# Kernel tuning notes

Measured on AMD Instinct MI355X. Metric: run time of the kernel, lower is better.

## Reference

```python
import jax, jax.numpy as jnp
import numpy as np

EPS = 1e-05  # matches tf entropy epsilon


def setup_inputs() -> dict:
    key = jax.random.key(0)
    k1, k2 = jax.random.split(key)
    encodings = jax.random.normal(k1, (8192, 64), dtype=jnp.float32)
    categorical = jax.random.uniform(k2, (8192, 25), dtype=jnp.float32)
    return {"encodings": encodings, "categorical": categorical, "k": 15}


def reference(encodings, categorical, k):
    B = encodings.shape[0]
    n_components = categorical.shape[1]
    k = min(k, B // 4)  # layer clamps k to batch_size // 4

    hard_groups = jnp.argmax(categorical, axis=1)           # [B] int
    max_groups = jnp.max(categorical, axis=1)               # [B]

    # Batched brute-force kNN. tf.norm's sqrt is monotonic, so the strict
    # comparison `dist < kth_dist` is identical on squared distances; working
    # in squared space avoids sqrt(0) issues and an extra pass.
    sq = jnp.sum(encodings * encodings, axis=1)             # [B]
    d2 = sq[:, None] + sq[None, :] - 2.0 * (encodings @ encodings.T)
    d2 = jnp.maximum(d2, 0.0)                               # [B, B]

    # (k+1)-smallest distances per row (0-indexed k, self-distance included,
    # matching tf.gather(tf.sort(distances), k)).
    neg_topk, _ = jax.lax.top_k(-d2, k + 1)                 # [B, k+1]
    kth = -neg_topk[:, k]                                   # [B] k-th smallest

    mask = (d2 < kth[:, None]).astype(jnp.float32)          # [B, B] strict <

    # Per-row label histogram over the neighborhood: counts[i,c] = #neighbors
    # of i in cluster c. Zero bins contribute 0 to -sum(b*log(b+eps)), same as
    # tf.bincount's variable-length output.
    onehot = jax.nn.one_hot(hard_groups, n_components, dtype=jnp.float32)
    counts = mask @ onehot                                  # [B, n_components]
    n_i = jnp.sum(counts, axis=-1, keepdims=True)           # [B, 1]
    bins = counts / jnp.maximum(n_i, 1.0)
    neighbourhood_entropy = -jnp.sum(bins * jnp.log(bins + EPS), axis=-1)  # [B]

    # Global cluster-size entropy + number of populated clusters.
    gcounts = jnp.sum(onehot, axis=0)                       # [n_components]
    gbins = gcounts / jnp.float32(B)
    cluster_size_entropy = -jnp.sum(gbins * jnp.log(gbins + EPS))
    n_populated = jnp.sum(gcounts > 0).astype(jnp.float32)

    return encodings, neighbourhood_entropy, cluster_size_entropy, n_populated, max_groups
```

## Files before the change

### kernel.cpp

```cpp
#include <hip/hip_runtime.h>
#include <math.h>

#define Bsz    8192
#define Dd     64
#define NC     25
#define RT     16
#define KCAP   16
#define EPSf   1e-5f
#define JMASK  2097151

typedef short  short8  __attribute__((ext_vector_type(8)));
typedef float  floatx4 __attribute__((ext_vector_type(4)));


__device__ inline unsigned short f2bf(float x) {
    unsigned u = __float_as_uint(x);
    u += 0x7FFFu + ((u >> 16) & 1u);
    return (unsigned short)(u >> 16);
}
__device__ inline float bf2f(unsigned short h) { return __uint_as_float(((unsigned)h) << 16); }

__device__ inline void oesort16(unsigned* a) {
    #pragma unroll
    for (int p = 1; p < 16; p <<= 1) {
        #pragma unroll
        for (int k = p; k >= 1; k >>= 1) {
            #pragma unroll
            for (int j = (k & (p - 1)); j + k < 16; j += 2 * k) {
                #pragma unroll
                for (int i = 0; i < k; ++i) {
                    if (i + j + k < 16 &&
                        ((i + j) / (2 * p)) == ((i + j + k) / (2 * p))) {
                        unsigned x = a[i + j], y = a[i + j + k];
                        a[i + j]     = (x < y) ? x : y;
                        a[i + j + k] = (x < y) ? y : x;
                    }
                }
            }
        }
    }
}
__device__ inline void bclean16(unsigned* t) {
    #pragma unroll
    for (int j = 8; j > 0; j >>= 1)
        #pragma unroll
        for (int i = 0; i < 16; ++i) {
            int l = i ^ j;
            if (l > i) {
                unsigned x = t[i], y = t[l];
                t[i] = (x < y) ? x : y;
                t[l] = (x < y) ? y : x;
            }
        }
}
__device__ inline void bmerge16(unsigned* ls, const unsigned* b) {
    unsigned t[16];
    #pragma unroll
    for (int i = 0; i < 16; ++i) { unsigned x = ls[i], y = b[15 - i]; t[i] = (x < y) ? x : y; }
    bclean16(t);
    #pragma unroll
    for (int i = 0; i < 16; ++i) ls[i] = t[i];
}
__device__ inline void bmerge16_shfl(unsigned* ls, int mask) {
    unsigned t[16];
    #pragma unroll
    for (int i = 0; i < 16; ++i) {
        unsigned pv = (unsigned)__shfl_xor((int)ls[15 - i], mask);
        unsigned x = ls[i];
        t[i] = (x < pv) ? x : pv;
    }
    bclean16(t);
    #pragma unroll
    for (int i = 0; i < 16; ++i) ls[i] = t[i];
}

struct TileR { short8 a0, a1, a2, a3; uint4 sv; };

__device__ __attribute__((always_inline)) inline void tile_load(
    TileR& T, const char* __restrict__ enc2, const unsigned* __restrict__ slab,
    int soff, int lane16, int quad4)
{
    const char* base = enc2 + soff + lane16;
    T.a0 = *(const short8*)(base);
    T.a1 = *(const short8*)(base + 1024);
    T.a2 = *(const short8*)(base + 2048);
    T.a3 = *(const short8*)(base + 3072);
    T.sv = *(const uint4*)(slab + (soff >> 8) + quad4);
}

__device__ __attribute__((always_inline)) inline void tile_mfma(
    const TileR& T, const short8* bh, const short8* bl, float sqi, unsigned* cand)
{
    floatx4 acc = (floatx4){0.f, 0.f, 0.f, 0.f};
    acc = __builtin_amdgcn_mfma_f32_16x16x32_bf16(T.a0, bh[0], acc, 0, 0, 0);
    acc = __builtin_amdgcn_mfma_f32_16x16x32_bf16(T.a0, bl[0], acc, 0, 0, 0);
    acc = __builtin_amdgcn_mfma_f32_16x16x32_bf16(T.a2, bh[0], acc, 0, 0, 0);
    acc = __builtin_amdgcn_mfma_f32_16x16x32_bf16(T.a1, bh[1], acc, 0, 0, 0);
    acc = __builtin_amdgcn_mfma_f32_16x16x32_bf16(T.a1, bl[1], acc, 0, 0, 0);
    acc = __builtin_amdgcn_mfma_f32_16x16x32_bf16(T.a3, bh[1], acc, 0, 0, 0);

    unsigned s[4] = {T.sv.x, T.sv.y, T.sv.z, T.sv.w};
    #pragma unroll
    for (int r = 0; r < 4; ++r) {
        float d2 = fmaxf(sqi + __uint_as_float(s[r] & ~31u) + acc[r], 0.f);
        cand[r] = (__float_as_uint(d2) & ~31u) | (s[r] & 31u);
    }
}


__global__ __launch_bounds__(256) void pre_kernel(
    const float* __restrict__ enc, const float* __restrict__ cat,
    unsigned int* __restrict__ slab,
    char* __restrict__ enc1, char* __restrict__ enc2,
    float* __restrict__ out_max, float* __restrict__ out_enc)
{
    const int gid = blockIdx.x * 256 + threadIdx.x;
    const int p = gid >> 5, pr = gid & 31;

    float2 ev = ((const float2*)enc)[gid];
    ((float2*)out_enc)[gid] = ev;

    float s = ev.x * ev.x + ev.y * ev.y;
    #pragma unroll
    for (int m = 1; m < 32; m <<= 1) s += __shfl_xor(s, m, 32);

    {
        const int g = p >> 4, c15p = p & 15;
        const int d0 = 2 * pr, kh = d0 >> 5, q = (d0 >> 3) & 3, e0 = d0 & 7;
        const int base = g * 4096 + kh * 1024 + (q * 16 + c15p) * 16 + e0 * 2;
        unsigned short ha = f2bf(ev.x), hb = f2bf(ev.y);
        unsigned short la = f2bf(ev.x - bf2f(ha)), lb = f2bf(ev.y - bf2f(hb));
        *(unsigned*)(enc1 + base)        = (unsigned)ha | ((unsigned)hb << 16);
        *(unsigned*)(enc1 + base + 2048) = (unsigned)la | ((unsigned)lb << 16);
        float y0 = -2.f * ev.x, y1 = -2.f * ev.y;
        unsigned short hc = f2bf(y0), hd = f2bf(y1);
        unsigned short lc = f2bf(y0 - bf2f(hc)), ld = f2bf(y1 - bf2f(hd));
        *(unsigned*)(enc2 + base)        = (unsigned)hc | ((unsigned)hd << 16);
        *(unsigned*)(enc2 + base + 2048) = (unsigned)lc | ((unsigned)ld << 16);
    }
    float cv = (pr < NC) ? cat[p * NC + pr] : -1.f;
    int ci = pr;
    #pragma unroll
    for (int m = 1; m < 32; m <<= 1) {
        float ov = __shfl_xor(cv, m, 32);
        int   oi = __shfl_xor(ci, m, 32);
        if (ov > cv || (ov == cv && oi < ci)) { cv = ov; ci = oi; }
    }
    if (pr == 0) {
        out_max[p] = cv;
        slab[p] = (__float_as_uint(s) & ~31u) | (unsigned)ci;
    }
}

__global__ __launch_bounds__(512) void main_kernel(
    const char* __restrict__ enc1, const char* __restrict__ enc2,
    const unsigned int* __restrict__ slab, const int* __restrict__ kptr,
    float* __restrict__ out_ent, float* __restrict__ out_glob)
{
    __shared__ unsigned wl[8 * 16 * 17];
    __shared__ int cnt[32];

    const int tid  = threadIdx.x, bid = blockIdx.x;
    const int wv   = tid >> 6, lane = tid & 63;
    const int quad = (tid >> 4) & 3, c15 = tid & 15;
    const int rowbase = bid * RT;
    const int lane16 = lane * 16, quad4 = quad * 4;

    short8 bh[2], bl[2];
    {
        const char* ib = enc1 + (size_t)bid * 4096 + lane16;
        bh[0] = *(const short8*)(ib);
        bh[1] = *(const short8*)(ib + 1024);
        bl[0] = *(const short8*)(ib + 2048);
        bl[1] = *(const short8*)(ib + 3072);
    }
    const float sqi = __uint_as_float(slab[rowbase + c15] & ~31u);

    unsigned ls[KCAP];
    #pragma unroll
    for (int q = 0; q < KCAP; ++q) ls[q] = 0xFFFFFFFFu;

    const int wvoff = wv * 4096;

    TileR A0, A1, B0, B1;
    tile_load(A0, enc2, slab, wvoff,          lane16, quad4);
    tile_load(A1, enc2, slab, wvoff + 32768,  lane16, quad4);

    #pragma unroll 1
    for (int p = 0; p < 32; p += 2) {
        unsigned cand[16];
        {
            const int o = (wvoff + (p + 1) * 65536) & JMASK;
            tile_load(B0, enc2, slab, o, lane16, quad4);
        }
        __builtin_amdgcn_sched_barrier(0);
        tile_mfma(A0, bh, bl, sqi, cand);
        {
            const int o = ((wvoff + (p + 1) * 65536) & JMASK) + 32768;
            tile_load(B1, enc2, slab, o, lane16, quad4);
        }
        __builtin_amdgcn_sched_barrier(0);
        tile_mfma(A1, bh, bl, sqi, cand + 4);
        {
            const int o = (wvoff + (p + 2) * 65536) & JMASK;
            tile_load(A0, enc2, slab, o, lane16, quad4);
        }
        __builtin_amdgcn_sched_barrier(0);
        tile_mfma(B0, bh, bl, sqi, cand + 8);
        {
            const int o = ((wvoff + (p + 2) * 65536) & JMASK) + 32768;
            tile_load(A1, enc2, slab, o, lane16, quad4);
        }
        __builtin_amdgcn_sched_barrier(0);
        tile_mfma(B1, bh, bl, sqi, cand + 12);
        oesort16(cand);
        bmerge16(ls, cand);
    }

    if (bid == 0) {
        if (tid < 32) cnt[tid] = 0;
        __syncthreads();
        for (int i = tid; i < Bsz; i += 512) atomicAdd(&cnt[slab[i] & 31u], 1);
        __syncthreads();
        if (tid == 0) {
            float gent = 0.f, npop = 0.f;
            for (int i = 0; i < NC; ++i) {
                int g = cnt[i];
                if (g > 0) {
                    npop += 1.f;
                    float gb = (float)g / (float)Bsz;
                    gent -= gb * logf(gb + EPSf);
                }
            }
            out_glob[0] = gent;
            out_glob[1] = npop;
        }
        __syncthreads();
    }

    bmerge16_shfl(ls, 16);
    bmerge16_shfl(ls, 32);
    if (quad == 0) {
        #pragma unroll
        for (int q = 0; q < KCAP; ++q) wl[(wv * 16 + c15) * 17 + q] = ls[q];
    }
    __syncthreads();
    if (wv == 0) {
        const int row = tid >> 2, sub = tid & 3;
        unsigned A[16], Bv[16];
        #pragma unroll
        for (int i = 0; i < 16; ++i) A[i]  = wl[((2 * sub)     * 16 + row) * 17 + i];
        #pragma unroll
        for (int i = 0; i < 16; ++i) Bv[i] = wl[((2 * sub + 1) * 16 + row) * 17 + i];
        bmerge16(A, Bv);
        bmerge16_shfl(A, 1);
        bmerge16_shfl(A, 2);

        int kk = kptr[0];
        if (kk > Bsz / 4) kk = Bsz / 4;
        if (kk > KCAP - 1) kk = KCAP - 1;

        unsigned kth = A[15];
        #pragma unroll
        for (int q = 0; q < 16; ++q) if (q == kk) kth = A[q];
        int nn = 0;
        #pragma unroll
        for (int t = 0; t < 15; ++t) nn += (t < kk && A[t] < kth) ? 1 : 0;

        float inv = 1.f / (float)((nn > 0) ? nn : 1);
        float part = 0.f;
        #pragma unroll
        for (int a4 = 0; a4 < 4; ++a4) {
            int a = sub + 4 * a4;
            if (a < nn) {
                int la = (int)(A[a] & 31u);
                int c = 0;
                #pragma unroll
                for (int b = 0; b < 15; ++b) c += (b < nn && (int)(A[b] & 31u) == la) ? 1 : 0;
                part -= inv * logf((float)c * inv + EPSf);
            }
        }
        part += __shfl_xor(part, 1);
        part += __shfl_xor(part, 2);
        if (sub == 0) out_ent[rowbase + row] = part;
    }
}

extern "C" void kernel_launch(void* const* d_in, const int* in_sizes, int n_in,
                              void* d_out, int out_size, void* d_ws, size_t ws_size,
                              hipStream_t stream)
{
    const float* enc  = (const float*)d_in[0];
    const float* cat  = (const float*)d_in[1];
    const int*   kptr = (const int*)d_in[2];
    float* out = (float*)d_out;

    unsigned int* slab = (unsigned int*)d_ws;
    char*         enc1 = (char*)d_ws + 32768;
    char*         enc2 = (char*)d_ws + 2129920;

    float* out_enc  = out;
    float* out_ent  = out + Bsz * Dd;
    float* out_glob = out + Bsz * Dd + Bsz;
    float* out_max  = out + Bsz * Dd + Bsz + 2;

    pre_kernel<<<1024, 256, 0, stream>>>(enc, cat, slab, enc1, enc2, out_max, out_enc);
    main_kernel<<<Bsz / RT, 512, 0, stream>>>(enc1, enc2, slab, kptr, out_ent, out_glob);
}
```

Measured before the change: 120.1 us.

## Split squared-norm/label slab, drop clamp via signed keys, stagger wave start offsets

Splits the packed norm+label slab into separate float and label arrays, so the inner loop no longer masks the low bits of the norm. It also drops the fmaxf clamp by switching the sort keys to signed ints, which order negative distances correctly. Each wave now starts at a rotated column offset and sleeps briefly before its first load, to spread memory traffic across waves. The cost is an extra vector load per tile and small startup sleeps.

```diff
diff --git a/kernel.cpp b/kernel.cpp
--- a/kernel.cpp
+++ b/kernel.cpp
@@ -8,6 +8,7 @@
 #define KCAP   16
 #define EPSf   1e-5f
 #define JMASK  2097151
+#define SENT   0x7FFFFFFF
 
 typedef short  short8  __attribute__((ext_vector_type(8)));
 typedef float  floatx4 __attribute__((ext_vector_type(4)));
@@ -20,7 +21,7 @@
 }
 __device__ inline float bf2f(unsigned short h) { return __uint_as_float(((unsigned)h) << 16); }
 
-__device__ inline void oesort16(unsigned* a) {
+__device__ inline void oesort16(int* a) {
     #pragma unroll
     for (int p = 1; p < 16; p <<= 1) {
         #pragma unroll
@@ -31,7 +32,7 @@
                 for (int i = 0; i < k; ++i) {
                     if (i + j + k < 16 &&
                         ((i + j) / (2 * p)) == ((i + j + k) / (2 * p))) {
-                        unsigned x = a[i + j], y = a[i + j + k];
+                        int x = a[i + j], y = a[i + j + k];
                         a[i + j]     = (x < y) ? x : y;
                         a[i + j + k] = (x < y) ? y : x;
                     }
@@ -40,33 +41,33 @@
         }
     }
 }
-__device__ inline void bclean16(unsigned* t) {
+__device__ inline void bclean16(int* t) {
     #pragma unroll
     for (int j = 8; j > 0; j >>= 1)
         #pragma unroll
         for (int i = 0; i < 16; ++i) {
             int l = i ^ j;
             if (l > i) {
-                unsigned x = t[i], y = t[l];
+                int x = t[i], y = t[l];
                 t[i] = (x < y) ? x : y;
                 t[l] = (x < y) ? y : x;
             }
         }
 }
-__device__ inline void bmerge16(unsigned* ls, const unsigned* b) {
-    unsigned t[16];
-    #pragma unroll
-    for (int i = 0; i < 16; ++i) { unsigned x = ls[i], y = b[15 - i]; t[i] = (x < y) ? x : y; }
+__device__ inline void bmerge16(int* ls, const int* b) {
+    int t[16];
+    #pragma unroll
+    for (int i = 0; i < 16; ++i) { int x = ls[i], y = b[15 - i]; t[i] = (x < y) ? x : y; }
     bclean16(t);
     #pragma unroll
     for (int i = 0; i < 16; ++i) ls[i] = t[i];
 }
-__device__ inline void bmerge16_shfl(unsigned* ls, int mask) {
-    unsigned t[16];
+__device__ inline void bmerge16_shfl(int* ls, int mask) {
+    int t[16];
     #pragma unroll
     for (int i = 0; i < 16; ++i) {
-        unsigned pv = (unsigned)__shfl_xor((int)ls[15 - i], mask);
-        unsigned x = ls[i];
+        int pv = __shfl_xor(ls[15 - i], mask);
+        int x = ls[i];
         t[i] = (x < pv) ? x : pv;
     }
     bclean16(t);
@@ -74,10 +75,11 @@
     for (int i = 0; i < 16; ++i) ls[i] = t[i];
 }
 
-struct TileR { short8 a0, a1, a2, a3; uint4 sv; };
+struct TileR { short8 a0, a1, a2, a3; floatx4 svf; uint4 svl; };
 
 __device__ __attribute__((always_inline)) inline void tile_load(
-    TileR& T, const char* __restrict__ enc2, const unsigned* __restrict__ slab,
+    TileR& T, const char* __restrict__ enc2,
+    const float* __restrict__ sqf, const unsigned* __restrict__ lab,
     int soff, int lane16, int quad4)
 {
     const char* base = enc2 + soff + lane16;
@@ -85,11 +87,13 @@
     T.a1 = *(const short8*)(base + 1024);
     T.a2 = *(const short8*)(base + 2048);
     T.a3 = *(const short8*)(base + 3072);
-    T.sv = *(const uint4*)(slab + (soff >> 8) + quad4);
+    const int idx = (soff >> 8) + quad4;
+    T.svf = *(const floatx4*)(sqf + idx);
+    T.svl = *(const uint4*)(lab + idx);
 }
 
 __device__ __attribute__((always_inline)) inline void tile_mfma(
-    const TileR& T, const short8* bh, const short8* bl, float sqi, unsigned* cand)
+    const TileR& T, const short8* bh, const short8* bl, float sqi, int* cand)
 {
     floatx4 acc = (floatx4){0.f, 0.f, 0.f, 0.f};
     acc = __builtin_amdgcn_mfma_f32_16x16x32_bf16(T.a0, bh[0], acc, 0, 0, 0);
@@ -99,18 +103,18 @@
     acc = __builtin_amdgcn_mfma_f32_16x16x32_bf16(T.a1, bl[1], acc, 0, 0, 0);
     acc = __builtin_amdgcn_mfma_f32_16x16x32_bf16(T.a3, bh[1], acc, 0, 0, 0);
 
-    unsigned s[4] = {T.sv.x, T.sv.y, T.sv.z, T.sv.w};
+    const unsigned l4[4] = {T.svl.x, T.svl.y, T.svl.z, T.svl.w};
     #pragma unroll
     for (int r = 0; r < 4; ++r) {
-        float d2 = fmaxf(sqi + __uint_as_float(s[r] & ~31u) + acc[r], 0.f);
-        cand[r] = (__float_as_uint(d2) & ~31u) | (s[r] & 31u);
+        float d2 = sqi + T.svf[r] + acc[r];
+        cand[r] = (int)((__float_as_uint(d2) & ~31u) | l4[r]);
     }
 }
 
 
 __global__ __launch_bounds__(256) void pre_kernel(
     const float* __restrict__ enc, const float* __restrict__ cat,
-    unsigned int* __restrict__ slab,
+    float* __restrict__ sqf, unsigned int* __restrict__ lab,
     char* __restrict__ enc1, char* __restrict__ enc2,
     float* __restrict__ out_max, float* __restrict__ out_enc)
 {
@@ -148,16 +152,18 @@
     }
     if (pr == 0) {
         out_max[p] = cv;
-        slab[p] = (__float_as_uint(s) & ~31u) | (unsigned)ci;
+        sqf[p] = __uint_as_float(__float_as_uint(s) & ~31u);
+        lab[p] = (unsigned)ci;
     }
 }
 
 __global__ __launch_bounds__(512) void main_kernel(
     const char* __restrict__ enc1, const char* __restrict__ enc2,
-    const unsigned int* __restrict__ slab, const int* __restrict__ kptr,
+    const float* __restrict__ sqf, const unsigned* __restrict__ lab,
+    const int* __restrict__ kptr,
     float* __restrict__ out_ent, float* __restrict__ out_glob)
 {
-    __shared__ unsigned wl[8 * 16 * 17];
+    __shared__ int wl[8 * 16 * 17];
     __shared__ int cnt[32];
 
     const int tid  = threadIdx.x, bid = blockIdx.x;
@@ -174,42 +180,48 @@
         bl[0] = *(const short8*)(ib + 2048);
         bl[1] = *(const short8*)(ib + 3072);
     }
-    const float sqi = __uint_as_float(slab[rowbase + c15] & ~31u);
-
-    unsigned ls[KCAP];
-    #pragma unroll
-    for (int q = 0; q < KCAP; ++q) ls[q] = 0xFFFFFFFFu;
+    const float sqi = sqf[rowbase + c15];
+
+    int ls[KCAP];
+    #pragma unroll
+    for (int q = 0; q < KCAP; ++q) ls[q] = SENT;
 
     const int wvoff = wv * 4096;
+    const int rot   = wv * 4;
+
+    for (int d = 0; d < wv; ++d) __builtin_amdgcn_s_sleep(1);
 
     TileR A0, A1, B0, B1;
-    tile_load(A0, enc2, slab, wvoff,          lane16, quad4);
-    tile_load(A1, enc2, slab, wvoff + 32768,  lane16, quad4);
+    {
+        const int o = (wvoff + rot * 65536) & JMASK;
+        tile_load(A0, enc2, sqf, lab, o,          lane16, quad4);
+        tile_load(A1, enc2, sqf, lab, o + 32768,  lane16, quad4);
+    }
 
     #pragma unroll 1
     for (int p = 0; p < 32; p += 2) {
-        unsigned cand[16];
+        int cand[16];
         {
-            const int o = (wvoff + (p + 1) * 65536) & JMASK;
-            tile_load(B0, enc2, slab, o, lane16, quad4);
+            const int o = (wvoff + (p + 1 + rot) * 65536) & JMASK;
+            tile_load(B0, enc2, sqf, lab, o, lane16, quad4);
         }
         __builtin_amdgcn_sched_barrier(0);
         tile_mfma(A0, bh, bl, sqi, cand);
         {
-            const int o = ((wvoff + (p + 1) * 65536) & JMASK) + 32768;
-            tile_load(B1, enc2, slab, o, lane16, quad4);
+            const int o = ((wvoff + (p + 1 + rot) * 65536) & JMASK) + 32768;
+            tile_load(B1, enc2, sqf, lab, o, lane16, quad4);
         }
         __builtin_amdgcn_sched_barrier(0);
         tile_mfma(A1, bh, bl, sqi, cand + 4);
         {
-            const int o = (wvoff + (p + 2) * 65536) & JMASK;
-            tile_load(A0, enc2, slab, o, lane16, quad4);
+            const int o = (wvoff + (p + 2 + rot) * 65536) & JMASK;
+            tile_load(A0, enc2, sqf, lab, o, lane16, quad4);
         }
         __builtin_amdgcn_sched_barrier(0);
         tile_mfma(B0, bh, bl, sqi, cand + 8);
         {
-            const int o = ((wvoff + (p + 2) * 65536) & JMASK) + 32768;
-            tile_load(A1, enc2, slab, o, lane16, quad4);
+            const int o = ((wvoff + (p + 2 + rot) * 65536) & JMASK) + 32768;
+            tile_load(A1, enc2, sqf, lab, o, lane16, quad4);
         }
         __builtin_amdgcn_sched_barrier(0);
         tile_mfma(B1, bh, bl, sqi, cand + 12);
@@ -220,7 +232,7 @@
     if (bid == 0) {
         if (tid < 32) cnt[tid] = 0;
         __syncthreads();
-        for (int i = tid; i < Bsz; i += 512) atomicAdd(&cnt[slab[i] & 31u], 1);
+        for (int i = tid; i < Bsz; i += 512) atomicAdd(&cnt[lab[i]], 1);
         __syncthreads();
         if (tid == 0) {
             float gent = 0.f, npop = 0.f;
@@ -247,7 +259,7 @@
     __syncthreads();
     if (wv == 0) {
         const int row = tid >> 2, sub = tid & 3;
-        unsigned A[16], Bv[16];
+        int A[16], Bv[16];
         #pragma unroll
         for (int i = 0; i < 16; ++i) A[i]  = wl[((2 * sub)     * 16 + row) * 17 + i];
         #pragma unroll
@@ -260,7 +272,7 @@
         if (kk > Bsz / 4) kk = Bsz / 4;
         if (kk > KCAP - 1) kk = KCAP - 1;
 
-        unsigned kth = A[15];
+        int kth = A[15];
         #pragma unroll
         for (int q = 0; q < 16; ++q) if (q == kk) kth = A[q];
         int nn = 0;
@@ -273,10 +285,10 @@
         for (int a4 = 0; a4 < 4; ++a4) {
             int a = sub + 4 * a4;
             if (a < nn) {
-                int la = (int)(A[a] & 31u);
+                int la = A[a] & 31;
                 int c = 0;
                 #pragma unroll
-                for (int b = 0; b < 15; ++b) c += (b < nn && (int)(A[b] & 31u) == la) ? 1 : 0;
+                for (int b = 0; b < 15; ++b) c += (b < nn && (A[b] & 31) == la) ? 1 : 0;
                 part -= inv * logf((float)c * inv + EPSf);
             }
         }
@@ -295,15 +307,16 @@
     const int*   kptr = (const int*)d_in[2];
     float* out = (float*)d_out;
 
-    unsigned int* slab = (unsigned int*)d_ws;
-    char*         enc1 = (char*)d_ws + 32768;
-    char*         enc2 = (char*)d_ws + 2129920;
+    float*        sqf  = (float*)d_ws;
+    unsigned int* lab  = (unsigned int*)((char*)d_ws + 32768);
+    char*         enc1 = (char*)d_ws + 65536;
+    char*         enc2 = (char*)d_ws + 2162688;
 
     float* out_enc  = out;
     float* out_ent  = out + Bsz * Dd;
     float* out_glob = out + Bsz * Dd + Bsz;
     float* out_max  = out + Bsz * Dd + Bsz + 2;
 
-    pre_kernel<<<1024, 256, 0, stream>>>(enc, cat, slab, enc1, enc2, out_max, out_enc);
-    main_kernel<<<Bsz / RT, 512, 0, stream>>>(enc1, enc2, slab, kptr, out_ent, out_glob);
-}
+    pre_kernel<<<1024, 256, 0, stream>>>(enc, cat, sqf, lab, enc1, enc2, out_max, out_enc);
+    main_kernel<<<Bsz / RT, 512, 0, stream>>>(enc1, enc2, sqf, lab, kptr, out_ent, out_glob);
+}
```

Result: no change. 121.8 us (+1.4%).

## Process two 16-row tiles per block to reuse column tile loads

Applied to the files above, without the earlier changes.

Each block now handles 32 query rows with two independent MFMA accumulators per loaded column tile, so encoding and slab loads are shared across twice as many rows. Top-k lists use signed int keys, which lets negative squared distances sort first and removes the fmaxf clamp. The final merge uses two waves. This halves the number of blocks and raises register pressure from the extra B fragments and second top-k list, which may reduce occupancy.

```diff
diff --git a/kernel.cpp b/kernel.cpp
--- a/kernel.cpp
+++ b/kernel.cpp
@@ -4,10 +4,11 @@
 #define Bsz    8192
 #define Dd     64
 #define NC     25
-#define RT     16
+#define RT     32
 #define KCAP   16
 #define EPSf   1e-5f
 #define JMASK  2097151
+#define SENT   0x7FFFFFFF
 
 typedef short  short8  __attribute__((ext_vector_type(8)));
 typedef float  floatx4 __attribute__((ext_vector_type(4)));
@@ -20,7 +21,7 @@
 }
 __device__ inline float bf2f(unsigned short h) { return __uint_as_float(((unsigned)h) << 16); }
 
-__device__ inline void oesort16(unsigned* a) {
+__device__ inline void oesort16(int* a) {
     #pragma unroll
     for (int p = 1; p < 16; p <<= 1) {
         #pragma unroll
@@ -31,7 +32,7 @@
                 for (int i = 0; i < k; ++i) {
                     if (i + j + k < 16 &&
                         ((i + j) / (2 * p)) == ((i + j + k) / (2 * p))) {
-                        unsigned x = a[i + j], y = a[i + j + k];
+                        int x = a[i + j], y = a[i + j + k];
                         a[i + j]     = (x < y) ? x : y;
                         a[i + j + k] = (x < y) ? y : x;
                     }
@@ -40,33 +41,33 @@
         }
     }
 }
-__device__ inline void bclean16(unsigned* t) {
+__device__ inline void bclean16(int* t) {
     #pragma unroll
     for (int j = 8; j > 0; j >>= 1)
         #pragma unroll
         for (int i = 0; i < 16; ++i) {
             int l = i ^ j;
             if (l > i) {
-                unsigned x = t[i], y = t[l];
+                int x = t[i], y = t[l];
                 t[i] = (x < y) ? x : y;
                 t[l] = (x < y) ? y : x;
             }
         }
 }
-__device__ inline void bmerge16(unsigned* ls, const unsigned* b) {
-    unsigned t[16];
-    #pragma unroll
-    for (int i = 0; i < 16; ++i) { unsigned x = ls[i], y = b[15 - i]; t[i] = (x < y) ? x : y; }
+__device__ inline void bmerge16(int* ls, const int* b) {
+    int t[16];
+    #pragma unroll
+    for (int i = 0; i < 16; ++i) { int x = ls[i], y = b[15 - i]; t[i] = (x < y) ? x : y; }
     bclean16(t);
     #pragma unroll
     for (int i = 0; i < 16; ++i) ls[i] = t[i];
 }
-__device__ inline void bmerge16_shfl(unsigned* ls, int mask) {
-    unsigned t[16];
+__device__ inline void bmerge16_shfl(int* ls, int mask) {
+    int t[16];
     #pragma unroll
     for (int i = 0; i < 16; ++i) {
-        unsigned pv = (unsigned)__shfl_xor((int)ls[15 - i], mask);
-        unsigned x = ls[i];
+        int pv = __shfl_xor(ls[15 - i], mask);
+        int x = ls[i];
         t[i] = (x < pv) ? x : pv;
     }
     bclean16(t);
@@ -88,22 +89,34 @@
     T.sv = *(const uint4*)(slab + (soff >> 8) + quad4);
 }
 
-__device__ __attribute__((always_inline)) inline void tile_mfma(
-    const TileR& T, const short8* bh, const short8* bl, float sqi, unsigned* cand)
-{
-    floatx4 acc = (floatx4){0.f, 0.f, 0.f, 0.f};
-    acc = __builtin_amdgcn_mfma_f32_16x16x32_bf16(T.a0, bh[0], acc, 0, 0, 0);
-    acc = __builtin_amdgcn_mfma_f32_16x16x32_bf16(T.a0, bl[0], acc, 0, 0, 0);
-    acc = __builtin_amdgcn_mfma_f32_16x16x32_bf16(T.a2, bh[0], acc, 0, 0, 0);
-    acc = __builtin_amdgcn_mfma_f32_16x16x32_bf16(T.a1, bh[1], acc, 0, 0, 0);
-    acc = __builtin_amdgcn_mfma_f32_16x16x32_bf16(T.a1, bl[1], acc, 0, 0, 0);
-    acc = __builtin_amdgcn_mfma_f32_16x16x32_bf16(T.a3, bh[1], acc, 0, 0, 0);
-
-    unsigned s[4] = {T.sv.x, T.sv.y, T.sv.z, T.sv.w};
+__device__ __attribute__((always_inline)) inline void tile_mfma2(
+    const TileR& T,
+    const short8* bh0, const short8* bl0, const short8* bh1, const short8* bl1,
+    float sqi0, float sqi1, int* c0, int* c1)
+{
+    floatx4 p = (floatx4){0.f, 0.f, 0.f, 0.f};
+    floatx4 q = (floatx4){0.f, 0.f, 0.f, 0.f};
+    p = __builtin_amdgcn_mfma_f32_16x16x32_bf16(T.a0, bh0[0], p, 0, 0, 0);
+    q = __builtin_amdgcn_mfma_f32_16x16x32_bf16(T.a0, bh1[0], q, 0, 0, 0);
+    p = __builtin_amdgcn_mfma_f32_16x16x32_bf16(T.a0, bl0[0], p, 0, 0, 0);
+    q = __builtin_amdgcn_mfma_f32_16x16x32_bf16(T.a0, bl1[0], q, 0, 0, 0);
+    p = __builtin_amdgcn_mfma_f32_16x16x32_bf16(T.a2, bh0[0], p, 0, 0, 0);
+    q = __builtin_amdgcn_mfma_f32_16x16x32_bf16(T.a2, bh1[0], q, 0, 0, 0);
+    p = __builtin_amdgcn_mfma_f32_16x16x32_bf16(T.a1, bh0[1], p, 0, 0, 0);
+    q = __builtin_amdgcn_mfma_f32_16x16x32_bf16(T.a1, bh1[1], q, 0, 0, 0);
+    p = __builtin_amdgcn_mfma_f32_16x16x32_bf16(T.a1, bl0[1], p, 0, 0, 0);
+    q = __builtin_amdgcn_mfma_f32_16x16x32_bf16(T.a1, bl1[1], q, 0, 0, 0);
+    p = __builtin_amdgcn_mfma_f32_16x16x32_bf16(T.a3, bh0[1], p, 0, 0, 0);
+    q = __builtin_amdgcn_mfma_f32_16x16x32_bf16(T.a3, bh1[1], q, 0, 0, 0);
+
+    const unsigned s4[4] = {T.sv.x, T.sv.y, T.sv.z, T.sv.w};
     #pragma unroll
     for (int r = 0; r < 4; ++r) {
-        float d2 = fmaxf(sqi + __uint_as_float(s[r] & ~31u) + acc[r], 0.f);
-        cand[r] = (__float_as_uint(d2) & ~31u) | (s[r] & 31u);
+        const unsigned sqb = s4[r] & ~31u, lb = s4[r] & 31u;
+        float d0 = sqi0 + __uint_as_float(sqb) + p[r];
+        c0[r] = (int)((__float_as_uint(d0) & ~31u) | lb);
+        float d1 = sqi1 + __uint_as_float(sqb) + q[r];
+        c1[r] = (int)((__float_as_uint(d1) & ~31u) | lb);
     }
 }
 
@@ -157,7 +170,7 @@
     const unsigned int* __restrict__ slab, const int* __restrict__ kptr,
     float* __restrict__ out_ent, float* __restrict__ out_glob)
 {
-    __shared__ unsigned wl[8 * 16 * 17];
+    __shared__ int wl[8 * 32 * 17];
     __shared__ int cnt[32];
 
     const int tid  = threadIdx.x, bid = blockIdx.x;
@@ -166,19 +179,24 @@
     const int rowbase = bid * RT;
     const int lane16 = lane * 16, quad4 = quad * 4;
 
-    short8 bh[2], bl[2];
+    short8 bh0[2], bl0[2], bh1[2], bl1[2];
     {
-        const char* ib = enc1 + (size_t)bid * 4096 + lane16;
-        bh[0] = *(const short8*)(ib);
-        bh[1] = *(const short8*)(ib + 1024);
-        bl[0] = *(const short8*)(ib + 2048);
-        bl[1] = *(const short8*)(ib + 3072);
-    }
-    const float sqi = __uint_as_float(slab[rowbase + c15] & ~31u);
-
-    unsigned ls[KCAP];
-    #pragma unroll
-    for (int q = 0; q < KCAP; ++q) ls[q] = 0xFFFFFFFFu;
+        const char* ib = enc1 + (size_t)bid * 8192 + lane16;
+        bh0[0] = *(const short8*)(ib);
+        bh0[1] = *(const short8*)(ib + 1024);
+        bl0[0] = *(const short8*)(ib + 2048);
+        bl0[1] = *(const short8*)(ib + 3072);
+        bh1[0] = *(const short8*)(ib + 4096);
+        bh1[1] = *(const short8*)(ib + 5120);
+        bl1[0] = *(const short8*)(ib + 6144);
+        bl1[1] = *(const short8*)(ib + 7168);
+    }
+    const float sqi0 = __uint_as_float(slab[rowbase + c15] & ~31u);
+    const float sqi1 = __uint_as_float(slab[rowbase + 16 + c15] & ~31u);
+
+    int ls0[KCAP], ls1[KCAP];
+    #pragma unroll
+    for (int q = 0; q < KCAP; ++q) { ls0[q] = SENT; ls1[q] = SENT; }
 
     const int wvoff = wv * 4096;
 
@@ -188,33 +206,35 @@
 
     #pragma unroll 1
     for (int p = 0; p < 32; p += 2) {
-        unsigned cand[16];
+        int c0[16], c1[16];
         {
             const int o = (wvoff + (p + 1) * 65536) & JMASK;
             tile_load(B0, enc2, slab, o, lane16, quad4);
         }
         __builtin_amdgcn_sched_barrier(0);
-        tile_mfma(A0, bh, bl, sqi, cand);
+        tile_mfma2(A0, bh0, bl0, bh1, bl1, sqi0, sqi1, c0, c1);
         {
             const int o = ((wvoff + (p + 1) * 65536) & JMASK) + 32768;
             tile_load(B1, enc2, slab, o, lane16, quad4);
         }
         __builtin_amdgcn_sched_barrier(0);
-        tile_mfma(A1, bh, bl, sqi, cand + 4);
+        tile_mfma2(A1, bh0, bl0, bh1, bl1, sqi0, sqi1, c0 + 4, c1 + 4);
         {
             const int o = (wvoff + (p + 2) * 65536) & JMASK;
             tile_load(A0, enc2, slab, o, lane16, quad4);
         }
         __builtin_amdgcn_sched_barrier(0);
-        tile_mfma(B0, bh, bl, sqi, cand + 8);
+        tile_mfma2(B0, bh0, bl0, bh1, bl1, sqi0, sqi1, c0 + 8, c1 + 8);
         {
             const int o = ((wvoff + (p + 2) * 65536) & JMASK) + 32768;
             tile_load(A1, enc2, slab, o, lane16, quad4);
         }
         __builtin_amdgcn_sched_barrier(0);
-        tile_mfma(B1, bh, bl, sqi, cand + 12);
-        oesort16(cand);
-        bmerge16(ls, cand);
+        tile_mfma2(B1, bh0, bl0, bh1, bl1, sqi0, sqi1, c0 + 12, c1 + 12);
+        oesort16(c0);
+        bmerge16(ls0, c0);
+        oesort16(c1);
+        bmerge16(ls1, c1);
     }
 
     if (bid == 0) {
@@ -238,20 +258,24 @@
         __syncthreads();
     }
 
-    bmerge16_shfl(ls, 16);
-    bmerge16_shfl(ls, 32);
+    bmerge16_shfl(ls0, 16);
+    bmerge16_shfl(ls0, 32);
+    bmerge16_shfl(ls1, 16);
+    bmerge16_shfl(ls1, 32);
     if (quad == 0) {
         #pragma unroll
-        for (int q = 0; q < KCAP; ++q) wl[(wv * 16 + c15) * 17 + q] = ls[q];
+        for (int q = 0; q < KCAP; ++q) wl[(wv * 32 + c15) * 17 + q]      = ls0[q];
+        #pragma unroll
+        for (int q = 0; q < KCAP; ++q) wl[(wv * 32 + 16 + c15) * 17 + q] = ls1[q];
     }
     __syncthreads();
-    if (wv == 0) {
+    if (wv < 2) {
         const int row = tid >> 2, sub = tid & 3;
-        unsigned A[16], Bv[16];
-        #pragma unroll
-        for (int i = 0; i < 16; ++i) A[i]  = wl[((2 * sub)     * 16 + row) * 17 + i];
-        #pragma unroll
-        for (int i = 0; i < 16; ++i) Bv[i] = wl[((2 * sub + 1) * 16 + row) * 17 + i];
+        int A[16], Bv[16];
+        #pragma unroll
+        for (int i = 0; i < 16; ++i) A[i]  = wl[((2 * sub)     * 32 + row) * 17 + i];
+        #pragma unroll
+        for (int i = 0; i < 16; ++i) Bv[i] = wl[((2 * sub + 1) * 32 + row) * 17 + i];
         bmerge16(A, Bv);
         bmerge16_shfl(A, 1);
         bmerge16_shfl(A, 2);
@@ -260,7 +284,7 @@
         if (kk > Bsz / 4) kk = Bsz / 4;
         if (kk > KCAP - 1) kk = KCAP - 1;
 
-        unsigned kth = A[15];
+        int kth = A[15];
         #pragma unroll
         for (int q = 0; q < 16; ++q) if (q == kk) kth = A[q];
         int nn = 0;
@@ -273,10 +297,10 @@
         for (int a4 = 0; a4 < 4; ++a4) {
             int a = sub + 4 * a4;
             if (a < nn) {
-                int la = (int)(A[a] & 31u);
+                int la = A[a] & 31;
                 int c = 0;
                 #pragma unroll
-                for (int b = 0; b < 15; ++b) c += (b < nn && (int)(A[b] & 31u) == la) ? 1 : 0;
+                for (int b = 0; b < 15; ++b) c += (b < nn && (A[b] & 31) == la) ? 1 : 0;
                 part -= inv * logf((float)c * inv + EPSf);
             }
         }
```

New measurement: 111.1 us (median of 2 runs). 1.08x faster.
